# Kernel tuning notes

Hardware: AMD Instinct MI355X
Metric: run time of the kernel (lower is better)

Reference implementation:

```python
import jax, jax.numpy as jnp
import numpy as np

NUM_HEADS = 4
KEY_DIM = 128


def rel_to_abs(rel):
    # rel: [B, heads, L, ww, 2*ww-1] -> [B, heads, L, ww, ww]
    B, heads, L, ww, dim = rel.shape
    flat = rel.reshape(B, heads, L, ww * (2 * ww - 1))[:, :, :, ww - 1:-1]
    return flat.reshape(B, heads, L, ww, 2 * (ww - 1))[..., :ww]


def relative_logits(pos_q, pos_emb_w, pos_emb_h):
    # pos_q: [B, hh, ww, heads, kd]
    # width logits
    q_w = jnp.transpose(pos_q, (0, 3, 1, 2, 4))           # [B, heads, hh, ww, kd]
    rel_w = jnp.einsum('bhxyd,dr->bhxyr', q_w, pos_emb_w)  # [B, heads, hh, ww, 2ww-1]
    rel_w = rel_to_abs(rel_w)                              # [B, heads, hh, ww, ww]
    # height logits
    q_h = jnp.transpose(pos_q, (0, 3, 2, 1, 4))           # [B, heads, ww, hh, kd]
    rel_h = jnp.einsum('bhyxd,dr->bhyxr', q_h, pos_emb_h)  # [B, heads, ww, hh, 2hh-1]
    rel_h = rel_to_abs(rel_h)                              # [B, heads, ww, hh, hh]
    rel_h = jnp.transpose(rel_h, (0, 1, 3, 2, 4))          # [B, heads, hh, ww, hh]
    # broadcast-add: [B, heads, hh, ww, hh, ww]
    return rel_w[:, :, :, :, None, :] + rel_h[:, :, :, :, :, None]


def setup_inputs() -> dict:
    key = jax.random.key(0)
    ks = jax.random.split(key, 7)
    B, H, W, C = 8, 32, 32, 512
    emb = NUM_HEADS * KEY_DIM
    stddev = KEY_DIM ** (-0.5)
    return {
        'x': jax.random.normal(ks[0], (B, H, W, C), jnp.float32),
        'Wq': jax.random.normal(ks[1], (C, emb), jnp.float32) * 0.02,
        'Wk': jax.random.normal(ks[2], (C, emb), jnp.float32) * 0.02,
        'Wv': jax.random.normal(ks[3], (C, emb), jnp.float32) * 0.02,
        'Wo': jax.random.normal(ks[4], (emb, emb), jnp.float32) * 0.02,
        'pos_emb_w': jax.random.normal(ks[5], (KEY_DIM, 2 * W - 1), jnp.float32) * stddev,
        'pos_emb_h': jax.random.normal(ks[6], (KEY_DIM, 2 * H - 1), jnp.float32) * stddev,
    }


def reference(x, Wq, Wk, Wv, Wo, pos_emb_w, pos_emb_h):
    B, hh, ww, C = x.shape
    heads, kd = NUM_HEADS, KEY_DIM
    L = hh * ww
    scale = 1.0 / jnp.sqrt(jnp.asarray(kd, x.dtype))

    q = (x @ Wq) * scale                                    # [B, hh, ww, heads*kd]
    attn_q = q.reshape(B, L, heads, kd).transpose(0, 2, 1, 3)   # [B, heads, L, kd]
    pos_q = q.reshape(B, hh, ww, heads, kd)
    k = (x @ Wk).reshape(B, L, heads, kd).transpose(0, 2, 3, 1)  # [B, heads, kd, L]
    v = (x @ Wv).reshape(B, L, heads, kd).transpose(0, 2, 1, 3)  # [B, heads, L, kd]

    scores = attn_q @ k                                      # [B, heads, L, L]
    pos = relative_logits(pos_q, pos_emb_w, pos_emb_h)        # [B, heads, hh, ww, hh, ww]
    scores = scores + pos.reshape(B, heads, L, L)
    attn = jax.nn.softmax(scores, axis=-1)

    out = attn @ v                                            # [B, heads, L, kd]
    out = out.transpose(0, 2, 1, 3).reshape(B, hh, ww, heads * kd)
    return out @ Wo
```

## Files before the change

kernel.cpp:

```cpp
#include <hip/hip_runtime.h>
#include <math.h>

typedef unsigned short u16;
typedef unsigned int u32;
typedef __bf16 bf16x8 __attribute__((ext_vector_type(8)));
typedef float f32x4 __attribute__((ext_vector_type(4)));

__device__ __forceinline__ u16 f2b(float f) {
  u32 u = __builtin_bit_cast(u32, f);
  u32 r = (u + 0x7FFFu + ((u >> 16) & 1u)) >> 16;
  return (u16)r;
}

__device__ __forceinline__ void glds16(const void* g, void* lds) {
  __builtin_amdgcn_global_load_lds(
      (const __attribute__((address_space(1))) void*)(void*)(const_cast<void*>(g)),
      (__attribute__((address_space(3))) void*)lds, 16, 0, 0);
}

#define QSCALE (0.08838834764831845f * 1.4426950408889634f)

__global__ __launch_bounds__(256) void prep_all(
    const float* __restrict__ x, const float* __restrict__ Wq, const float* __restrict__ Wk,
    const float* __restrict__ Wv, const float* __restrict__ Wo,
    const float* __restrict__ pew, const float* __restrict__ peh,
    u16* __restrict__ xb, u16* __restrict__ WbigT, u16* __restrict__ WoT)
{
  __shared__ float wrow[512];
  const int bid = blockIdx.x;
  const int t = threadIdx.x;
  if (bid < 4096) {
    int idx = bid * 256 + t;
    float4 v = ((const float4*)x)[idx];
    ushort4 o;
    o.x = f2b(v.x); o.y = f2b(v.y); o.z = f2b(v.z); o.w = f2b(v.w);
    ((ushort4*)xb)[idx] = o;
  } else if (bid < 6152) {
    int row = bid - 4096;
    if (row < 512) {
      for (int k = t; k < 512; k += 256) WbigT[row*512 + k] = f2b(Wq[k*512 + row] * QSCALE);
    } else if (row < 1024) {
      int n = row - 512;
      for (int k = t; k < 512; k += 256) WbigT[row*512 + k] = f2b(Wk[k*512 + n]);
    } else if (row < 1536) {
      int n = row - 1024;
      for (int k = t; k < 512; k += 256) WbigT[row*512 + k] = f2b(Wv[k*512 + n]);
    } else if (row < 1544) {
      int rr = row - 1536 + 2040;
      for (int k = t; k < 512; k += 256) WbigT[rr*512 + k] = 0;
    } else {
      int n = row - 1544;
      for (int k = t; k < 512; k += 256) WoT[n*512 + k] = f2b(Wo[k*512 + n]);
    }
  } else {
    int k = bid - 6152;
    for (int j = t; j < 512; j += 256) wrow[j] = Wq[k*512 + j];
    __syncthreads();
    if (t < 252) {
      int h = t / 63, r = t - h*63;
      float aw = 0.f, ah = 0.f;
      for (int d = 0; d < 128; d++) {
        float qv = wrow[h*128 + d];
        aw += qv * pew[d*63 + r];
        ah += qv * peh[d*63 + r];
      }
      WbigT[(size_t)(1536 + t)*512 + k] = f2b(aw * QSCALE);
      WbigT[(size_t)(1788 + t)*512 + k] = f2b(ah * QSCALE);
    }
  }
}

__global__ __launch_bounds__(512) void gemm256(
    const u16* __restrict__ A, const u16* __restrict__ Bt,
    u16* __restrict__ Qb, u16* __restrict__ Kb, u16* __restrict__ Vt,
    float* __restrict__ RELW, float* __restrict__ RELH)
{
  __shared__ char sm[131072];
  const int tid = threadIdx.x;
  const int w = tid >> 6, l = tid & 63, g = l >> 4, c = l & 15;
  const int bm = blockIdx.x, bn = blockIdx.y;
  const int wm = w >> 2, wn = w & 3;

  f32x4 acc[8][4];
#pragma unroll
  for (int i = 0; i < 8; i++)
#pragma unroll
    for (int j = 0; j < 4; j++) acc[i][j] = f32x4{0.f, 0.f, 0.f, 0.f};

  const char* Ab = (const char*)A;
  const char* Bb = (const char*)Bt;
  const int rsub = l >> 3;
  const int csw = (((l & 7) ^ rsub) << 4);

#define A_STAGE(kb, p)                                                                    \
  {                                                                                       \
    char* As_ = sm + (p)*65536;                                                           \
    const int kbyte = (kb) * 128;                                                         \
    _Pragma("unroll")                                                                     \
    for (int i2 = 0; i2 < 4; i2++) {                                                      \
      const int row = i2*64 + w*8 + rsub;                                                 \
      glds16(Ab + (size_t)(bm*256 + row) * 1024 + kbyte + csw, As_ + i2*8192 + w*1024);   \
    }                                                                                     \
  }
#define B_STAGE(kb, p)                                                                    \
  {                                                                                       \
    char* Bs_ = sm + (p)*65536 + 32768;                                                   \
    const int kbyte = (kb) * 128;                                                         \
    _Pragma("unroll")                                                                     \
    for (int i2 = 0; i2 < 4; i2++) {                                                      \
      const int row = i2*64 + w*8 + rsub;                                                 \
      glds16(Bb + (size_t)(bn*256 + row) * 1024 + kbyte + csw, Bs_ + i2*8192 + w*1024);   \
    }                                                                                     \
  }

  B_STAGE(0, 0); A_STAGE(0, 0);
  B_STAGE(1, 1); A_STAGE(1, 1);

#pragma unroll
  for (int kb = 0; kb < 8; kb++) {
    const int p = kb & 1;
    if (kb == 0)      { asm volatile("s_waitcnt vmcnt(8)" ::: "memory"); }
    else if (kb < 7)  { asm volatile("s_waitcnt vmcnt(4)" ::: "memory"); }
    else              { asm volatile("s_waitcnt vmcnt(0)" ::: "memory"); }
    __builtin_amdgcn_s_barrier();

    const char* As_ = sm + p*65536;
    const char* Bs_ = As_ + 32768;

    bf16x8 bf[4][2], af[4][2];
#pragma unroll
    for (int ks = 0; ks < 2; ks++) {
      const int koff = (ks*64 + g*16) ^ ((c & 7) << 4);
#pragma unroll
      for (int mf = 0; mf < 4; mf++)
        af[mf][ks] = *(const bf16x8*)(As_ + (wm*128 + mf*16 + c)*128 + koff);
#pragma unroll
      for (int nf = 0; nf < 4; nf++)
        bf[nf][ks] = *(const bf16x8*)(Bs_ + (wn*64 + nf*16 + c)*128 + koff);
    }
    if (kb >= 1 && kb < 7) A_STAGE(kb + 1, p ^ 1);
    __builtin_amdgcn_s_setprio(1);
#pragma unroll
    for (int ks = 0; ks < 2; ks++)
#pragma unroll
      for (int mf = 0; mf < 4; mf++)
#pragma unroll
        for (int nf = 0; nf < 4; nf++)
          acc[mf][nf] = __builtin_amdgcn_mfma_f32_16x16x32_bf16(af[mf][ks], bf[nf][ks], acc[mf][nf], 0, 0, 0);
    __builtin_amdgcn_s_setprio(0);
    __builtin_amdgcn_s_barrier();

#pragma unroll
    for (int ks = 0; ks < 2; ks++) {
      const int koff = (ks*64 + g*16) ^ ((c & 7) << 4);
#pragma unroll
      for (int mf = 0; mf < 4; mf++)
        af[mf][ks] = *(const bf16x8*)(As_ + (wm*128 + (mf + 4)*16 + c)*128 + koff);
    }
    if (kb < 6) B_STAGE(kb + 2, p);
    __builtin_amdgcn_s_setprio(1);
#pragma unroll
    for (int ks = 0; ks < 2; ks++)
#pragma unroll
      for (int mf = 0; mf < 4; mf++)
#pragma unroll
        for (int nf = 0; nf < 4; nf++)
          acc[mf + 4][nf] = __builtin_amdgcn_mfma_f32_16x16x32_bf16(af[mf][ks], bf[nf][ks], acc[mf + 4][nf], 0, 0, 0);
    __builtin_amdgcn_s_setprio(0);
    __builtin_amdgcn_s_barrier();
  }
#undef A_STAGE
#undef B_STAGE

  const int b = bm >> 2;
  const int iBase = (bm & 3) * 256;

  if (bn < 4) {
    u16* dst0 = (bn < 2) ? Qb : Kb;
    const int bnn = bn & 1;
#pragma unroll
    for (int mf = 0; mf < 8; mf++) {
      const int lmb = wm*128 + mf*16 + g*4;
#pragma unroll
      for (int nf = 0; nf < 4; nf++) {
        const int ln = wn*64 + nf*16 + c;
#pragma unroll
        for (int r = 0; r < 4; r++) {
          const int lm = lmb + r;
          *(u16*)(sm + lm*512 + ((ln*2) ^ ((lm & 7) << 4))) = f2b(acc[mf][nf][r]);
        }
      }
    }
    __builtin_amdgcn_s_barrier();
#pragma unroll
    for (int it = 0; it < 16; it++) {
      const int gid = it*512 + tid;
      const int lm2 = gid >> 5, gsub = gid & 31;
      bf16x8 v = *(const bf16x8*)(sm + lm2*512 + ((gsub*16) ^ ((lm2 & 7) << 4)));
      const int h = bnn*2 + (gsub >> 4);
      const int d0 = (gsub & 15) * 8;
      *(bf16x8*)(dst0 + ((size_t)(b*4 + h)*1024 + iBase + lm2)*128 + d0) = v;
    }
  } else if (bn < 6) {
#pragma unroll
    for (int mf = 0; mf < 8; mf++) {
      const int lmb = wm*128 + mf*16 + g*4;
#pragma unroll
      for (int nf = 0; nf < 4; nf++) {
        const int ln = wn*64 + nf*16 + c;
        u32 w0, w1;
        asm("v_cvt_pk_bf16_f32 %0, %1, %2" : "=v"(w0) : "v"(acc[mf][nf][0]), "v"(acc[mf][nf][1]));
        asm("v_cvt_pk_bf16_f32 %0, %1, %2" : "=v"(w1) : "v"(acc[mf][nf][2]), "v"(acc[mf][nf][3]));
        uint2 pk; pk.x = w0; pk.y = w1;
        *(uint2*)(sm + ln*512 + ((lmb*2) ^ ((c & 7) << 4))) = pk;
      }
    }
    __builtin_amdgcn_s_barrier();
#pragma unroll
    for (int it = 0; it < 16; it++) {
      const int gid = it*512 + tid;
      const int ln2 = gid >> 5, gsub = gid & 31;
      bf16x8 v = *(const bf16x8*)(sm + ln2*512 + ((gsub*16) ^ ((ln2 & 7) << 4)));
      const int q2 = (bn - 4)*256 + ln2;
      const int h = q2 >> 7, d = q2 & 127;
      *(bf16x8*)(Vt + ((size_t)(b*4 + h)*128 + d)*1024 + iBase + gsub*8) = v;
    }
  } else {
#pragma unroll
    for (int mf = 0; mf < 8; mf++) {
      const int lmb = wm*128 + mf*16 + g*4;
#pragma unroll
      for (int nf = 0; nf < 4; nf++) {
        const int q = (bn - 6)*256 + wn*64 + nf*16 + c;
        if (q < 252) {
          const int h = q / 63, r2 = q - h*63;
#pragma unroll
          for (int r = 0; r < 4; r++)
            RELW[(size_t)((b*4 + h)*1024 + iBase + lmb + r)*64 + r2] = acc[mf][nf][r];
        } else if (q < 504) {
          const int qq = q - 252;
          const int h = qq / 63, r2 = qq - h*63;
#pragma unroll
          for (int r = 0; r < 4; r++)
            RELH[(size_t)((b*4 + h)*1024 + iBase + lmb + r)*64 + r2] = acc[mf][nf][r];
        }
      }
    }
  }
}

__global__ __launch_bounds__(512) void attn_fused(
    const u16* __restrict__ Qb, const u16* __restrict__ Kb, const u16* __restrict__ Vt,
    const float* __restrict__ RELW, const float* __restrict__ RELH,
    u16* __restrict__ AO)
{
  __shared__ char sm[81920];
  char* const Pl = sm + 65536;
  const int tid = threadIdx.x;
  const int w = tid >> 6, l = tid & 63, g = l >> 4, c = l & 15;
  const int bh = blockIdx.x, qt = blockIdx.y;
  const int i0 = qt * 128;

  bf16x8 qf[4];
  {
    const char* qbase = (const char*)Qb + (size_t)(bh*1024 + i0 + w*16 + c) * 256;
#pragma unroll
    for (int s = 0; s < 4; s++) qf[s] = *(const bf16x8*)(qbase + s*64 + g*16);
  }

  const int i = i0 + w*16 + c;
  const int xi = i & 31, yi = i >> 5;
  const float* rw = RELW + ((size_t)(bh*1024 + i) << 6);
  const float* rhb = RELH + ((size_t)(bh*1024 + i) << 6) + (31 - yi);
  float xwh[2][4];
#pragma unroll
  for (int e = 0; e < 2; e++)
#pragma unroll
    for (int r = 0; r < 4; r++) xwh[e][r] = rw[e*16 + g*4 + r - xi + 31];

  f32x4 Oacc[8];
#pragma unroll
  for (int fd = 0; fd < 8; fd++) Oacc[fd] = f32x4{0.f, 0.f, 0.f, 0.f};
  float m_q = -INFINITY, l_q = 0.f;

#define A_STAGE(jt, p)                                                                     \
  {                                                                                        \
    char* Kt_ = sm + (p)*16384;                                                            \
    char* Vs_ = sm + 32768 + (p)*16384;                                                    \
    const int j0b = (jt) * 64;                                                             \
    _Pragma("unroll")                                                                      \
    for (int t = 0; t < 2; t++) {                                                          \
      const int L = (w*2 + t)*1024 + l*16;                                                 \
      const int jr = L >> 8, jb = L & 255;                                                 \
      glds16((const char*)Kb + (size_t)(bh*1024 + j0b + jr) * 256 + (jb ^ ((jr & 7) << 4)),\
             Kt_ + L);                                                                     \
      const int dr = L >> 7, db = L & 127;                                                 \
      glds16((const char*)Vt + (size_t)(bh*128 + dr) * 2048 + j0b*2 + (db ^ ((dr & 7) << 4)),\
             Vs_ + L);                                                                     \
    }                                                                                      \
  }

  float yh0 = rhb[0], yh1 = rhb[1];
  asm volatile("" ::: "memory");
  A_STAGE(0, 0);
  A_STAGE(1, 1);

#pragma unroll 2
  for (int jt = 0; jt < 16; jt++) {
    const int p = jt & 1;
    if (jt < 15) { asm volatile("s_waitcnt vmcnt(4)" ::: "memory"); }
    else         { asm volatile("s_waitcnt vmcnt(0)" ::: "memory"); }
    __builtin_amdgcn_s_barrier();

    const char* Kt_ = sm + p*16384;
    const char* Vs_ = sm + 32768 + p*16384;

    f32x4 acc[4];
#pragma unroll
    for (int fn = 0; fn < 4; fn++) acc[fn] = f32x4{0.f, 0.f, 0.f, 0.f};
    __builtin_amdgcn_s_setprio(1);
#pragma unroll
    for (int s = 0; s < 4; s++) {
      const int koff = (s*64 + g*16) ^ ((c & 7) << 4);
#pragma unroll
      for (int fn = 0; fn < 4; fn++) {
        bf16x8 kf = *(const bf16x8*)(Kt_ + (fn*16 + c)*256 + koff);
        acc[fn] = __builtin_amdgcn_mfma_f32_16x16x32_bf16(kf, qf[s], acc[fn], 0, 0, 0);
      }
    }
    __builtin_amdgcn_s_setprio(0);

#pragma unroll
    for (int fn = 0; fn < 4; fn++)
#pragma unroll
      for (int r = 0; r < 4; r++)
        acc[fn][r] += xwh[fn & 1][r] + ((fn >> 1) ? yh1 : yh0);

    float mx = fmaxf(fmaxf(fmaxf(acc[0][0], acc[0][1]), fmaxf(acc[0][2], acc[0][3])),
                     fmaxf(fmaxf(acc[1][0], acc[1][1]), fmaxf(acc[1][2], acc[1][3])));
    mx = fmaxf(mx, fmaxf(fmaxf(fmaxf(acc[2][0], acc[2][1]), fmaxf(acc[2][2], acc[2][3])),
                         fmaxf(fmaxf(acc[3][0], acc[3][1]), fmaxf(acc[3][2], acc[3][3]))));
    mx = fmaxf(mx, __shfl_xor(mx, 16));
    mx = fmaxf(mx, __shfl_xor(mx, 32));

    if (__any(mx > m_q + 8.f)) {
      const float mnew = fmaxf(m_q, mx);
      const float scq = exp2f(m_q - mnew);
      m_q = mnew;
      l_q *= scq;
#pragma unroll
      for (int r = 0; r < 4; r++) {
        const float scr = __shfl(scq, g*4 + r, 16);
#pragma unroll
        for (int fd = 0; fd < 8; fd++) Oacc[fd][r] *= scr;
      }
    }

    float pv[4][4];
    float ps = 0.f;
#pragma unroll
    for (int fn = 0; fn < 4; fn++) {
#pragma unroll
      for (int r = 0; r < 4; r++) {
        pv[fn][r] = exp2f(acc[fn][r] - m_q);
        ps += pv[fn][r];
      }
    }
    ps += __shfl_xor(ps, 16);
    ps += __shfl_xor(ps, 32);
    l_q += ps;

    float nyh0 = 0.f, nyh1 = 0.f;
    if (jt < 15) { nyh0 = rhb[(jt + 1)*2]; nyh1 = rhb[(jt + 1)*2 + 1]; }

    {
      char* pb = Pl + w*2048 + c*128;
      const int swz = (c & 7) << 4;
#pragma unroll
      for (int fn = 0; fn < 4; fn++) {
        u32 w0, w1;
        asm("v_cvt_pk_bf16_f32 %0, %1, %2" : "=v"(w0) : "v"(pv[fn][0]), "v"(pv[fn][1]));
        asm("v_cvt_pk_bf16_f32 %0, %1, %2" : "=v"(w1) : "v"(pv[fn][2]), "v"(pv[fn][3]));
        uint2 pk; pk.x = w0; pk.y = w1;
        *(uint2*)(pb + ((fn*32 + g*8) ^ swz)) = pk;
      }
    }

    __builtin_amdgcn_s_setprio(1);
#pragma unroll
    for (int s = 0; s < 2; s++) {
      const int koff = (s*64 + g*16) ^ ((c & 7) << 4);
      bf16x8 pf = *(const bf16x8*)(Pl + w*2048 + c*128 + koff);
#pragma unroll
      for (int fd = 0; fd < 8; fd++) {
        bf16x8 vf = *(const bf16x8*)(Vs_ + (fd*16 + c)*128 + koff);
        Oacc[fd] = __builtin_amdgcn_mfma_f32_16x16x32_bf16(pf, vf, Oacc[fd], 0, 0, 0);
      }
    }
    __builtin_amdgcn_s_setprio(0);

    __builtin_amdgcn_s_barrier();
    if (jt < 14) A_STAGE(jt + 2, p);
    yh0 = nyh0; yh1 = nyh1;
  }
#undef A_STAGE

  const int b = bh >> 2, h = bh & 3;
#pragma unroll
  for (int r = 0; r < 4; r++) {
    const float lr = __shfl(l_q, g*4 + r, 16);
    const float linv = 1.0f / lr;
    const int io = i0 + w*16 + g*4 + r;
#pragma unroll
    for (int fd = 0; fd < 8; fd++) {
      AO[(size_t)(b*1024 + io)*512 + h*128 + fd*16 + c] = f2b(Oacc[fd][r] * linv);
    }
  }
}

__global__ __launch_bounds__(256) void gemm_out(
    const u16* __restrict__ A, const u16* __restrict__ Bt, float* __restrict__ outF)
{
  __shared__ char sm[65536];
  const int tid = threadIdx.x;
  const int w = tid >> 6, l = tid & 63, g = l >> 4, c = l & 15;
  const int bm = blockIdx.x, bn = blockIdx.y;
  const int wm = (w >> 1) * 64, wn = (w & 1) * 64;

  f32x4 acc[4][4];
#pragma unroll
  for (int i = 0; i < 4; i++)
#pragma unroll
    for (int j = 0; j < 4; j++) acc[i][j] = f32x4{0.f, 0.f, 0.f, 0.f};

  const char* Ab = (const char*)A;
  const char* Bb = (const char*)Bt;
  const int rsub = l >> 3;
  const int csw = (((l & 7) ^ rsub) << 4);

#define G_STAGE(kb, p)                                                                    \
  {                                                                                       \
    char* As_ = sm + (p)*32768;                                                           \
    char* Bs_ = As_ + 16384;                                                              \
    const int kbyte = (kb) * 128;                                                         \
    _Pragma("unroll")                                                                     \
    for (int t = 0; t < 4; t++) {                                                         \
      const int row = (w*4 + t)*8 + rsub;                                                 \
      glds16(Ab + (size_t)(bm*128 + row) * 1024 + kbyte + csw, As_ + (w*4 + t)*1024);     \
      glds16(Bb + (size_t)(bn*128 + row) * 1024 + kbyte + csw, Bs_ + (w*4 + t)*1024);     \
    }                                                                                     \
  }

  G_STAGE(0, 0);
  G_STAGE(1, 1);

#pragma unroll
  for (int kb = 0; kb < 8; kb++) {
    const int p = kb & 1;
    if (kb < 7) { asm volatile("s_waitcnt vmcnt(8)" ::: "memory"); }
    else        { asm volatile("s_waitcnt vmcnt(0)" ::: "memory"); }
    __builtin_amdgcn_s_barrier();
    const char* As_ = sm + p*32768;
    const char* Bs_ = As_ + 16384;
#pragma unroll
    for (int ks = 0; ks < 2; ks++) {
      const int koff = (ks*64 + g*16) ^ ((c & 7) << 4);
      bf16x8 af[4], bfr[4];
#pragma unroll
      for (int mf = 0; mf < 4; mf++)
        af[mf] = *(const bf16x8*)(As_ + (wm + mf*16 + c)*128 + koff);
#pragma unroll
      for (int nf = 0; nf < 4; nf++)
        bfr[nf] = *(const bf16x8*)(Bs_ + (wn + nf*16 + c)*128 + koff);
#pragma unroll
      for (int mf = 0; mf < 4; mf++)
#pragma unroll
        for (int nf = 0; nf < 4; nf++)
          acc[mf][nf] = __builtin_amdgcn_mfma_f32_16x16x32_bf16(af[mf], bfr[nf], acc[mf][nf], 0, 0, 0);
    }
    __builtin_amdgcn_s_barrier();
    if (kb < 6) G_STAGE(kb + 2, p);
  }
#undef G_STAGE

#pragma unroll
  for (int mf = 0; mf < 4; mf++) {
#pragma unroll
    for (int nf = 0; nf < 4; nf++) {
      const int n = bn*128 + wn + nf*16 + c;
#pragma unroll
      for (int r = 0; r < 4; r++) {
        const int m = bm*128 + wm + mf*16 + g*4 + r;
        outF[(size_t)m*512 + n] = acc[mf][nf][r];
      }
    }
  }
}

extern "C" void kernel_launch(void* const* d_in, const int* in_sizes, int n_in,
                              void* d_out, int out_size, void* d_ws, size_t ws_size,
                              hipStream_t stream) {
  const float* x   = (const float*)d_in[0];
  const float* Wq  = (const float*)d_in[1];
  const float* Wk  = (const float*)d_in[2];
  const float* Wv  = (const float*)d_in[3];
  const float* Wo  = (const float*)d_in[4];
  const float* pew = (const float*)d_in[5];
  const float* peh = (const float*)d_in[6];

  char* ws = (char*)d_ws;
  u16* xb    = (u16*)ws;    ws += (size_t)8192*512*2;
  u16* WbigT = (u16*)ws;    ws += (size_t)2048*512*2;
  u16* WoT   = (u16*)ws;    ws += (size_t)512*512*2;
  u16* Qb    = (u16*)ws;    ws += (size_t)32*1024*128*2;
  u16* Kb    = (u16*)ws;    ws += (size_t)32*1024*128*2;
  u16* Vt    = (u16*)ws;    ws += (size_t)32*1024*128*2;
  float* RELW = (float*)ws; ws += (size_t)32*1024*64*4;
  float* RELH = (float*)ws; ws += (size_t)32*1024*64*4;
  u16* AO    = (u16*)ws;    ws += (size_t)8192*512*2;

  prep_all<<<6664, 256, 0, stream>>>(x, Wq, Wk, Wv, Wo, pew, peh, xb, WbigT, WoT);
  gemm256<<<dim3(32, 8), 512, 0, stream>>>(xb, WbigT, Qb, Kb, Vt, RELW, RELH);
  attn_fused<<<dim3(32, 8), 512, 0, stream>>>(Qb, Kb, Vt, RELW, RELH, AO);
  gemm_out<<<dim3(64, 4), 256, 0, stream>>>(AO, WoT, (float*)d_out);
}
```

Baseline: 97.42 us.

## Split attention over key halves with flash-decoding style merge kernel

Splits the attention kernel along the key dimension into two halves, doubling the grid from 256 to 512 blocks so more CUs are occupied. Each half writes unnormalized bf16 partial outputs plus per-row max and sum, and a new merge kernel combines them in place into the first half's buffer. The output GEMM now reads the per-head [bh, L, 128] layout directly. This adds a kernel launch, extra global traffic for the partials, and a second bf16 rounding of the unnormalized output.

```diff
diff --git a/kernel.cpp b/kernel.cpp
--- a/kernel.cpp
+++ b/kernel.cpp
@@ -10,6 +10,11 @@
   u32 u = __builtin_bit_cast(u32, f);
   u32 r = (u + 0x7FFFu + ((u >> 16) & 1u)) >> 16;
   return (u16)r;
+}
+
+__device__ __forceinline__ float b2f(u16 b) {
+  u32 u = ((u32)b) << 16;
+  return __builtin_bit_cast(float, u);
 }
 
 __device__ __forceinline__ void glds16(const void* g, void* lds) {
@@ -249,17 +254,19 @@
   }
 }
 
-__global__ __launch_bounds__(512) void attn_fused(
+__global__ __launch_bounds__(512) void attn_split(
     const u16* __restrict__ Qb, const u16* __restrict__ Kb, const u16* __restrict__ Vt,
     const float* __restrict__ RELW, const float* __restrict__ RELH,
-    u16* __restrict__ AO)
+    u16* __restrict__ Opart, float2* __restrict__ ML)
 {
   __shared__ char sm[81920];
   char* const Pl = sm + 65536;
   const int tid = threadIdx.x;
   const int w = tid >> 6, l = tid & 63, g = l >> 4, c = l & 15;
-  const int bh = blockIdx.x, qt = blockIdx.y;
+  const int bh = blockIdx.x;
+  const int qt = blockIdx.y & 7, half = blockIdx.y >> 3;
   const int i0 = qt * 128;
+  const int jt0 = half * 8;
 
   bf16x8 qf[4];
   {
@@ -300,16 +307,17 @@
     }                                                                                      \
   }
 
-  float yh0 = rhb[0], yh1 = rhb[1];
+  float yh0 = rhb[jt0*2], yh1 = rhb[jt0*2 + 1];
   asm volatile("" ::: "memory");
-  A_STAGE(0, 0);
-  A_STAGE(1, 1);
+  A_STAGE(jt0, 0);
+  A_STAGE(jt0 + 1, 1);
 
 #pragma unroll 2
-  for (int jt = 0; jt < 16; jt++) {
-    const int p = jt & 1;
-    if (jt < 15) { asm volatile("s_waitcnt vmcnt(4)" ::: "memory"); }
-    else         { asm volatile("s_waitcnt vmcnt(0)" ::: "memory"); }
+  for (int jj = 0; jj < 8; jj++) {
+    const int jt = jt0 + jj;
+    const int p = jj & 1;
+    if (jj < 7) { asm volatile("s_waitcnt vmcnt(4)" ::: "memory"); }
+    else        { asm volatile("s_waitcnt vmcnt(0)" ::: "memory"); }
     __builtin_amdgcn_s_barrier();
 
     const char* Kt_ = sm + p*16384;
@@ -371,7 +379,7 @@
     l_q += ps;
 
     float nyh0 = 0.f, nyh1 = 0.f;
-    if (jt < 15) { nyh0 = rhb[(jt + 1)*2]; nyh1 = rhb[(jt + 1)*2 + 1]; }
+    if (jj < 7) { nyh0 = rhb[(jt + 1)*2]; nyh1 = rhb[(jt + 1)*2 + 1]; }
 
     {
       char* pb = Pl + w*2048 + c*128;
@@ -400,21 +408,53 @@
     __builtin_amdgcn_s_setprio(0);
 
     __builtin_amdgcn_s_barrier();
-    if (jt < 14) A_STAGE(jt + 2, p);
+    if (jj < 6) A_STAGE(jt + 2, p);
     yh0 = nyh0; yh1 = nyh1;
   }
 #undef A_STAGE
 
-  const int b = bh >> 2, h = bh & 3;
-#pragma unroll
-  for (int r = 0; r < 4; r++) {
-    const float lr = __shfl(l_q, g*4 + r, 16);
-    const float linv = 1.0f / lr;
-    const int io = i0 + w*16 + g*4 + r;
-#pragma unroll
-    for (int fd = 0; fd < 8; fd++) {
-      AO[(size_t)(b*1024 + io)*512 + h*128 + fd*16 + c] = f2b(Oacc[fd][r] * linv);
-    }
+  const size_t rbase = (size_t)(half*32 + bh)*1024;
+#pragma unroll
+  for (int fd = 0; fd < 8; fd++) {
+#pragma unroll
+    for (int r = 0; r < 4; r++) {
+      const int io = i0 + w*16 + g*4 + r;
+      Opart[(rbase + io)*128 + fd*16 + c] = f2b(Oacc[fd][r]);
+    }
+  }
+  if (l < 16) {
+    float2 s2; s2.x = m_q; s2.y = l_q;
+    ML[rbase + i0 + w*16 + l] = s2;
+  }
+}
+
+__global__ __launch_bounds__(256) void attn_merge(
+    u16* __restrict__ Opart, const float2* __restrict__ ML)
+{
+  const int bh = blockIdx.x, qb = blockIdx.y;
+  const int t = threadIdx.x;
+  const int row = t >> 3, dg = t & 7;
+  const int i = qb*32 + row;
+  const size_t r0 = (size_t)bh*1024 + i;
+  const size_t r1 = (size_t)(32 + bh)*1024 + i;
+  const float2 ml0 = ML[r0], ml1 = ML[r1];
+  const float m = fmaxf(ml0.x, ml1.x);
+  const float w0 = exp2f(ml0.x - m), w1 = exp2f(ml1.x - m);
+  const float linv = 1.0f / (ml0.y*w0 + ml1.y*w1);
+  u16* p0 = Opart + r0*128 + dg*16;
+  const u16* p1 = Opart + r1*128 + dg*16;
+#pragma unroll
+  for (int hlf = 0; hlf < 2; hlf++) {
+    bf16x8 a = *(const bf16x8*)(p0 + hlf*8);
+    bf16x8 b = *(const bf16x8*)(p1 + hlf*8);
+    u16 outv[8];
+#pragma unroll
+    for (int e = 0; e < 8; e++) {
+      float va = b2f(((const u16*)&a)[e]);
+      float vb = b2f(((const u16*)&b)[e]);
+      outv[e] = f2b((va*w0 + vb*w1) * linv);
+    }
+    *(bf16x8*)(p0 + hlf*8) = *(const bf16x8*)outv;
   }
 }
 
@@ -437,17 +477,21 @@
   const char* Bb = (const char*)Bt;
   const int rsub = l >> 3;
   const int csw = (((l & 7) ^ rsub) << 4);
+  const int b_ = bm >> 3;
+  const int iT = (bm & 7) * 128;
 
 #define G_STAGE(kb, p)                                                                    \
   {                                                                                       \
     char* As_ = sm + (p)*32768;                                                           \
     char* Bs_ = As_ + 16384;                                                              \
-    const int kbyte = (kb) * 128;                                                         \
+    const int h_ = (kb) >> 1;                                                             \
+    const int dof = ((kb) & 1) * 128;                                                     \
     _Pragma("unroll")                                                                     \
     for (int t = 0; t < 4; t++) {                                                         \
       const int row = (w*4 + t)*8 + rsub;                                                 \
-      glds16(Ab + (size_t)(bm*128 + row) * 1024 + kbyte + csw, As_ + (w*4 + t)*1024);     \
-      glds16(Bb + (size_t)(bn*128 + row) * 1024 + kbyte + csw, Bs_ + (w*4 + t)*1024);     \
+      glds16(Ab + (size_t)((b_*4 + h_)*1024 + iT + row) * 256 + dof + csw,                \
+             As_ + (w*4 + t)*1024);                                                       \
+      glds16(Bb + (size_t)(bn*128 + row) * 1024 + (kb)*128 + csw, Bs_ + (w*4 + t)*1024);  \
     }                                                                                     \
   }
 
@@ -517,10 +561,12 @@
   u16* Vt    = (u16*)ws;    ws += (size_t)32*1024*128*2;
   float* RELW = (float*)ws; ws += (size_t)32*1024*64*4;
   float* RELH = (float*)ws; ws += (size_t)32*1024*64*4;
-  u16* AO    = (u16*)ws;    ws += (size_t)8192*512*2;
+  u16* Opart = (u16*)ws;    ws += (size_t)2*32*1024*128*2;
+  float2* MLb = (float2*)ws; ws += (size_t)2*32*1024*8;
 
   prep_all<<<6664, 256, 0, stream>>>(x, Wq, Wk, Wv, Wo, pew, peh, xb, WbigT, WoT);
   gemm256<<<dim3(32, 8), 512, 0, stream>>>(xb, WbigT, Qb, Kb, Vt, RELW, RELH);
-  attn_fused<<<dim3(32, 8), 512, 0, stream>>>(Qb, Kb, Vt, RELW, RELH, AO);
-  gemm_out<<<dim3(64, 4), 256, 0, stream>>>(AO, WoT, (float*)d_out);
-}
+  attn_split<<<dim3(32, 16), 512, 0, stream>>>(Qb, Kb, Vt, RELW, RELH, Opart, MLb);
+  attn_merge<<<dim3(32, 32), 256, 0, stream>>>(Opart, MLb);
+  gemm_out<<<dim3(64, 4), 256, 0, stream>>>(Opart, WoT, (float*)d_out);
+}
```

New measurement: 106.8 us. 1.1x slower.

## Split projection GEMM main loop into quarter-phases with finer-grained async staging

Applied to the files above, without the earlier changes.

Restructures the QKV projection GEMM K-loop into four sub-phases per k-block. Each phase loads two A fragments and issues half-stage global-to-LDS loads for the next tiles, with a barrier pair around each MFMA cluster. The aim is to interleave memory loads more evenly with compute and cut register pressure from A fragments. In exchange it adds more barriers per k-block, and the hand-tuned vmcnt waits and buffer reuse ordering risk correctness if any count is off.

```diff
diff --git a/kernel.cpp b/kernel.cpp
--- a/kernel.cpp
+++ b/kernel.cpp
@@ -92,85 +92,86 @@
   const int rsub = l >> 3;
   const int csw = (((l & 7) ^ rsub) << 4);
 
-#define A_STAGE(kb, p)                                                                    \
+#define SA(kb, h, p)                                                                      \
   {                                                                                       \
     char* As_ = sm + (p)*65536;                                                           \
     const int kbyte = (kb) * 128;                                                         \
     _Pragma("unroll")                                                                     \
-    for (int i2 = 0; i2 < 4; i2++) {                                                      \
+    for (int i2 = (h)*2; i2 < (h)*2 + 2; i2++) {                                          \
       const int row = i2*64 + w*8 + rsub;                                                 \
       glds16(Ab + (size_t)(bm*256 + row) * 1024 + kbyte + csw, As_ + i2*8192 + w*1024);   \
     }                                                                                     \
   }
-#define B_STAGE(kb, p)                                                                    \
+#define SB(kb, h, p)                                                                      \
   {                                                                                       \
     char* Bs_ = sm + (p)*65536 + 32768;                                                   \
     const int kbyte = (kb) * 128;                                                         \
     _Pragma("unroll")                                                                     \
-    for (int i2 = 0; i2 < 4; i2++) {                                                      \
+    for (int i2 = (h)*2; i2 < (h)*2 + 2; i2++) {                                          \
       const int row = i2*64 + w*8 + rsub;                                                 \
       glds16(Bb + (size_t)(bn*256 + row) * 1024 + kbyte + csw, Bs_ + i2*8192 + w*1024);   \
     }                                                                                     \
   }
 
-  B_STAGE(0, 0); A_STAGE(0, 0);
-  B_STAGE(1, 1); A_STAGE(1, 1);
-
-#pragma unroll
-  for (int kb = 0; kb < 8; kb++) {
-    const int p = kb & 1;
-    if (kb == 0)      { asm volatile("s_waitcnt vmcnt(8)" ::: "memory"); }
-    else if (kb < 7)  { asm volatile("s_waitcnt vmcnt(4)" ::: "memory"); }
-    else              { asm volatile("s_waitcnt vmcnt(0)" ::: "memory"); }
-    __builtin_amdgcn_s_barrier();
-
-    const char* As_ = sm + p*65536;
-    const char* Bs_ = As_ + 32768;
-
-    bf16x8 bf[4][2], af[4][2];
-#pragma unroll
-    for (int ks = 0; ks < 2; ks++) {
-      const int koff = (ks*64 + g*16) ^ ((c & 7) << 4);
-#pragma unroll
-      for (int mf = 0; mf < 4; mf++)
-        af[mf][ks] = *(const bf16x8*)(As_ + (wm*128 + mf*16 + c)*128 + koff);
-#pragma unroll
-      for (int nf = 0; nf < 4; nf++)
-        bf[nf][ks] = *(const bf16x8*)(Bs_ + (wn*64 + nf*16 + c)*128 + koff);
-    }
-    if (kb >= 1 && kb < 7) A_STAGE(kb + 1, p ^ 1);
-    __builtin_amdgcn_s_setprio(1);
-#pragma unroll
-    for (int ks = 0; ks < 2; ks++)
-#pragma unroll
-      for (int mf = 0; mf < 4; mf++)
-#pragma unroll
-        for (int nf = 0; nf < 4; nf++)
-          acc[mf][nf] = __builtin_amdgcn_mfma_f32_16x16x32_bf16(af[mf][ks], bf[nf][ks], acc[mf][nf], 0, 0, 0);
-    __builtin_amdgcn_s_setprio(0);
-    __builtin_amdgcn_s_barrier();
-
-#pragma unroll
-    for (int ks = 0; ks < 2; ks++) {
-      const int koff = (ks*64 + g*16) ^ ((c & 7) << 4);
-#pragma unroll
-      for (int mf = 0; mf < 4; mf++)
-        af[mf][ks] = *(const bf16x8*)(As_ + (wm*128 + (mf + 4)*16 + c)*128 + koff);
-    }
-    if (kb < 6) B_STAGE(kb + 2, p);
-    __builtin_amdgcn_s_setprio(1);
-#pragma unroll
-    for (int ks = 0; ks < 2; ks++)
-#pragma unroll
-      for (int mf = 0; mf < 4; mf++)
-#pragma unroll
-        for (int nf = 0; nf < 4; nf++)
-          acc[mf + 4][nf] = __builtin_amdgcn_mfma_f32_16x16x32_bf16(af[mf][ks], bf[nf][ks], acc[mf + 4][nf], 0, 0, 0);
-    __builtin_amdgcn_s_setprio(0);
-    __builtin_amdgcn_s_barrier();
-  }
-#undef A_STAGE
-#undef B_STAGE
+  SB(0, 0, 0); SB(0, 1, 0); SA(0, 0, 0); SA(0, 1, 0);
+  SB(1, 0, 1); SB(1, 1, 1);
+  asm volatile("s_waitcnt vmcnt(4)" ::: "memory");
+  __builtin_amdgcn_s_barrier();
+
+  bf16x8 bf[4][2];
+
+#pragma unroll
+  for (int I = 0; I < 4; I++) {
+#pragma unroll
+    for (int ts = 0; ts < 2; ts++) {
+      const int p = ts;
+      const char* As_ = sm + p*65536;
+      const char* Bs_ = As_ + 32768;
+#pragma unroll
+      for (int q = 0; q < 4; q++) {
+        bf16x8 af[2][2];
+#pragma unroll
+        for (int ks = 0; ks < 2; ks++) {
+          const int koff = (ks*64 + g*16) ^ ((c & 7) << 4);
+          if (q == 0) {
+#pragma unroll
+            for (int nf = 0; nf < 4; nf++)
+              bf[nf][ks] = *(const bf16x8*)(Bs_ + (wn*64 + nf*16 + c)*128 + koff);
+          }
+#pragma unroll
+          for (int mi = 0; mi < 2; mi++)
+            af[mi][ks] = *(const bf16x8*)(As_ + (wm*128 + (q*2 + mi)*16 + c)*128 + koff);
+        }
+        if (ts == 0) {
+          if (q == 0) SA(2*I + 1, 0, 1);
+          if (q == 1) SA(2*I + 1, 1, 1);
+          if (q == 2 && I < 3) SB(2*I + 2, 0, 0);
+          if (q == 3) {
+            if (I < 3) { SB(2*I + 2, 1, 0); asm volatile("s_waitcnt vmcnt(4)" ::: "memory"); }
+            else       { asm volatile("s_waitcnt vmcnt(0)" ::: "memory"); }
+          }
+        } else {
+          if (q == 0 && I < 3) SA(2*I + 2, 0, 0);
+          if (q == 1 && I < 3) SA(2*I + 2, 1, 0);
+          if (q == 2 && I < 3) SB(2*I + 3, 0, 1);
+          if (q == 3 && I < 3) { SB(2*I + 3, 1, 1); asm volatile("s_waitcnt vmcnt(4)" ::: "memory"); }
+        }
+        __builtin_amdgcn_s_barrier();
+        __builtin_amdgcn_s_setprio(1);
+#pragma unroll
+        for (int ks = 0; ks < 2; ks++)
+#pragma unroll
+          for (int mi = 0; mi < 2; mi++)
+#pragma unroll
+            for (int nf = 0; nf < 4; nf++)
+              acc[q*2 + mi][nf] = __builtin_amdgcn_mfma_f32_16x16x32_bf16(af[mi][ks], bf[nf][ks], acc[q*2 + mi][nf], 0, 0, 0);
+        __builtin_amdgcn_s_setprio(0);
+        __builtin_amdgcn_s_barrier();
+      }
+    }
+  }
+#undef SA
+#undef SB
 
   const int b = bm >> 2;
   const int iBase = (bm & 3) * 256;
```

After: 97.78 us. About the same (+0.4%).
